# Kernel tuning notes

Hardware: AMD Instinct MI355X
Metric: run time of the kernel (lower is better)

Reference implementation:

```python
import jax, jax.numpy as jnp
import numpy as np

N_NODES = 50000
N_EDGES = 1600000
N_GRAPHS = 512
IN_C, H1, H2, H3, OUT_C = 16, 64, 64, 128, 10


def setup_inputs() -> dict:
    key = jax.random.key(0)
    ks = jax.random.split(key, 12)
    x = jax.random.normal(ks[0], (N_NODES, IN_C), dtype=jnp.float32)
    edge_index = jax.random.randint(ks[1], (2, N_EDGES), 0, N_NODES, dtype=jnp.int64 if jax.config.jax_enable_x64 else jnp.int32)
    batch = jnp.sort(jax.random.randint(ks[2], (N_NODES,), 0, N_GRAPHS))
    s = 0.05
    return {
        "x": x,
        "edge_index": edge_index,
        "batch": batch,
        "W1": jax.random.normal(ks[3], (IN_C, H1), dtype=jnp.float32) * s,
        "b1": jnp.zeros((H1,), jnp.float32),
        "W2": jax.random.normal(ks[4], (H1, H2), dtype=jnp.float32) * s,
        "b2": jnp.zeros((H2,), jnp.float32),
        "Wf1": jax.random.normal(ks[5], (H2, H3), dtype=jnp.float32) * s,
        "bf1": jnp.zeros((H3,), jnp.float32),
        "Wf2": jax.random.normal(ks[6], (H3, OUT_C), dtype=jnp.float32) * s,
        "bf2": jnp.zeros((OUT_C,), jnp.float32),
    }


def reference(x, edge_index, batch, W1, b1, W2, b2, Wf1, bf1, Wf2, bf2):
    N = x.shape[0]
    self_idx = jnp.arange(N, dtype=edge_index.dtype)
    # PyG GCNConv default: add self-loops, symmetric normalization deg^-1/2
    src = jnp.concatenate([edge_index[0], self_idx])
    dst = jnp.concatenate([edge_index[1], self_idx])
    deg = jnp.zeros((N,), x.dtype).at[dst].add(1.0)  # >= 1 due to self-loops
    dinv = jax.lax.rsqrt(deg)
    norm = dinv[src] * dinv[dst]  # [E+N]

    def gcn_conv(h, W, b):
        hw = h @ W                                   # [N, C_out]
        msgs = hw[src] * norm[:, None]               # gather [E+N, C_out]
        return jax.ops.segment_sum(msgs, dst, num_segments=N) + b

    h = jax.nn.relu(gcn_conv(x, W1, b1))
    h = jax.nn.relu(gcn_conv(h, W2, b2))

    # global_mean_pool over graph ids
    counts = jax.ops.segment_sum(jnp.ones((N,), h.dtype), batch, num_segments=N_GRAPHS)
    sums = jax.ops.segment_sum(h, batch, num_segments=N_GRAPHS)
    pooled = sums / jnp.maximum(counts, 1.0)[:, None]  # [G, H2]

    out = pooled @ Wf1 + bf1
    out = out @ Wf2 + bf2
    return out
```

## Files before the change

kernel.cpp:

```cpp
#include <hip/hip_runtime.h>

#define N_NODES   50000
#define N_EDGES   1600000
#define N_GRAPHS  512
#define IN_C      16
#define H1        64
#define H2        64
#define H3        128
#define OUT_C     10

#define NBKT      196
#define CHUNK     4096
#define CAP       12288
#define PLANE_DW  (N_NODES * 16)

typedef unsigned int  uint;
typedef unsigned short ushort;


__global__ void __launch_bounds__(256) k_binB(const int* __restrict__ src,
                                              const int* __restrict__ dst,
                                              int* __restrict__ bkt_fill,
                                              uint* __restrict__ bucket_edges) {
    __shared__ int  lcnt[NBKT];
    __shared__ int  loff[NBKT];
    __shared__ int  gbase[NBKT];
    __shared__ int  tmp[256];
    __shared__ uint stage[CHUNK];
    int tid = threadIdx.x;
    long long e0 = (long long)blockIdx.x * CHUNK;
    int cn = (int)((N_EDGES - e0) < CHUNK ? (N_EDGES - e0) : CHUNK);

    for (int i = tid; i < NBKT; i += 256) lcnt[i] = 0;
    __syncthreads();

    uint pk[16]; int rk[16]; int bkr[16];
#pragma unroll
    for (int k = 0; k < 16; ++k) {
        int i = k * 256 + tid;
        pk[k] = 0; rk[k] = -1; bkr[k] = 0;
        if (i < cn) {
            int e = (int)e0 + i;
            uint d = (uint)dst[e], s = (uint)src[e];
            pk[k] = (d << 16) | s;
            bkr[k] = (int)(d >> 8);
            rk[k] = atomicAdd(&lcnt[bkr[k]], 1);
        }
    }
    __syncthreads();

    int v = (tid < NBKT) ? lcnt[tid] : 0;
    tmp[tid] = v;
    __syncthreads();
    for (int s = 1; s < 256; s <<= 1) {
        int t = (tid >= s) ? tmp[tid - s] : 0;
        __syncthreads();
        tmp[tid] += t;
        __syncthreads();
    }
    if (tid < NBKT) loff[tid] = tmp[tid] - v;
    if (tid < NBKT && v > 0) gbase[tid] = atomicAdd(&bkt_fill[tid], v);
    __syncthreads();

#pragma unroll
    for (int k = 0; k < 16; ++k)
        if (rk[k] >= 0) stage[loff[bkr[k]] + rk[k]] = pk[k];
    __syncthreads();

    for (int i = tid; i < cn; i += 256) {
        uint p = stage[i];
        int b = (int)(p >> 24);
        int pos = gbase[b] + (i - loff[b]);
        if (pos < CAP) bucket_edges[(size_t)b * CAP + pos] = p;
    }
}


__global__ void __launch_bounds__(256) k_bkt_csr(const int* __restrict__ bkt_fill,
                                                 const uint* __restrict__ bucket_edges,
                                                 const float* __restrict__ x,
                                                 int* __restrict__ rowbeg,
                                                 int* __restrict__ rowend,
                                                 float* __restrict__ dinv,
                                                 float* __restrict__ xs,
                                                 ushort* __restrict__ src_sorted,
                                                 float* __restrict__ pool,
                                                 float* __restrict__ gcnt) {
    __shared__ int ncnt[256];
    __shared__ int noff[256];
    __shared__ int tmp[256];
    __shared__ ushort su[CAP];
    int b = blockIdx.x, tid = threadIdx.x;
    int base = b * CAP;
    int cntE = bkt_fill[b];
    if (cntE > CAP) cntE = CAP;

    int gt = b * 256 + tid;
    if (gt < N_GRAPHS * H2) pool[gt] = 0.f;
    if (gt < N_GRAPHS) gcnt[gt] = 0.f;

    ncnt[tid] = 0;
    __syncthreads();
    for (int i = tid; i < cntE; i += 256) {
        uint p = bucket_edges[base + i];
        atomicAdd(&ncnt[(p >> 16) & 255], 1);
    }
    __syncthreads();

    int v = ncnt[tid];
    tmp[tid] = v;
    __syncthreads();
    for (int s = 1; s < 256; s <<= 1) {
        int t = (tid >= s) ? tmp[tid - s] : 0;
        __syncthreads();
        tmp[tid] += t;
        __syncthreads();
    }
    noff[tid] = tmp[tid] - v;

    int n = b * 256 + tid;
    if (n < N_NODES) {
        rowbeg[n] = base + (tmp[tid] - v);
        rowend[n] = base + tmp[tid];
        float dv = rsqrtf((float)(v + 1));
        dinv[n] = dv;
        const float4* xr = (const float4*)(x + (size_t)n * IN_C);
        float4* xo = (float4*)(xs + (size_t)n * IN_C);
#pragma unroll
        for (int j = 0; j < 4; ++j) {
            float4 t = xr[j];
            t.x *= dv; t.y *= dv; t.z *= dv; t.w *= dv;
            xo[j] = t;
        }
    }

    ncnt[tid] = 0;
    __syncthreads();
    for (int i = tid; i < cntE; i += 256) {
        uint p = bucket_edges[base + i];
        int l = (p >> 16) & 255;
        int r = atomicAdd(&ncnt[l], 1);
        int pos = noff[l] + r;
        if (pos < CAP) su[pos] = (ushort)(p & 0xFFFF);
    }
    __syncthreads();
    for (int i = tid; i < cntE; i += 256)
        src_sorted[base + i] = su[i];
}


__device__ __forceinline__ uint f2bf(float f) {
    uint b = __float_as_uint(f);
    return (b + 0x7fffu + ((b >> 16) & 1u)) >> 16;
}

__global__ void __launch_bounds__(256) k_layer1(
    const int* __restrict__ rowbeg, const int* __restrict__ rowend,
    const ushort* __restrict__ src_sorted,
    const float* __restrict__ dinv, const float* __restrict__ xs,
    const float* __restrict__ W1, const float* __restrict__ b1,
    const float* __restrict__ W2, uint* __restrict__ ubf)
{
    __shared__ float W1l[IN_C * 64];
    __shared__ float W2l[H1 * 64];
    __shared__ float axl[32 * 16];
    __shared__ float tl[32 * 64];
    int tid = threadIdx.x;

    ((float4*)W1l)[tid] = ((const float4*)W1)[tid];
#pragma unroll
    for (int i = tid; i < H1 * 16; i += 256)
        ((float4*)W2l)[i] = ((const float4*)W2)[i];

    int ln = tid >> 3;
    int n = blockIdx.x * 32 + ln;
    int sub = tid & 7;
    int slot = sub >> 2;
    int c4 = (sub & 3) << 2;
    bool valid = n < N_NODES;

    int beg = 0, end = 0;
    float di = 0.f;
    if (valid) { beg = rowbeg[n]; end = rowend[n]; di = dinv[n]; }

    float4 acc = {0.f,0.f,0.f,0.f}, acc2 = {0.f,0.f,0.f,0.f};
    if (valid && slot == 0)
        acc = *(const float4*)(xs + (size_t)n * 16 + c4);

    for (int i = beg; i < end; i += 4) {
        int i0 = i + slot, i1 = i0 + 2;
        bool k0 = i0 < end, k1 = i1 < end;
        int s0 = k0 ? (int)src_sorted[i0] : 0;
        int s1 = k1 ? (int)src_sorted[i1] : 0;
        float m0 = k0 ? 1.f : 0.f;
        float m1 = k1 ? 1.f : 0.f;
        float4 h0 = *(const float4*)(xs + (size_t)s0 * 16 + c4);
        float4 h1 = *(const float4*)(xs + (size_t)s1 * 16 + c4);
        acc.x  = fmaf(h0.x, m0, acc.x);   acc.y  = fmaf(h0.y, m0, acc.y);
        acc.z  = fmaf(h0.z, m0, acc.z);   acc.w  = fmaf(h0.w, m0, acc.w);
        acc2.x = fmaf(h1.x, m1, acc2.x);  acc2.y = fmaf(h1.y, m1, acc2.y);
        acc2.z = fmaf(h1.z, m1, acc2.z);  acc2.w = fmaf(h1.w, m1, acc2.w);
    }
    acc.x += acc2.x; acc.y += acc2.y; acc.z += acc2.z; acc.w += acc2.w;
    acc.x += __shfl_xor(acc.x, 4);
    acc.y += __shfl_xor(acc.y, 4);
    acc.z += __shfl_xor(acc.z, 4);
    acc.w += __shfl_xor(acc.w, 4);
    if (slot == 0) {
        acc.x *= di; acc.y *= di; acc.z *= di; acc.w *= di;
        *(float4*)(&axl[ln * 16 + c4]) = acc;
    }
    __syncthreads();

    int c0 = (tid & 7) * 8;
    float a1[8];
#pragma unroll
    for (int j = 0; j < 8; ++j) a1[j] = 0.f;
    const float* an = &axl[ln * 16];
#pragma unroll
    for (int kb = 0; kb < IN_C / 4; ++kb) {
        float4 r = *(const float4*)(an + kb * 4);
        const float* wr = &W1l[(kb * 4) * 64 + c0];
        float rk[4] = {r.x, r.y, r.z, r.w};
#pragma unroll
        for (int k = 0; k < 4; ++k) {
            float4 w0 = *(const float4*)(wr + k * 64);
            float4 w1 = *(const float4*)(wr + k * 64 + 4);
            a1[0] += rk[k] * w0.x;  a1[1] += rk[k] * w0.y;
            a1[2] += rk[k] * w0.z;  a1[3] += rk[k] * w0.w;
            a1[4] += rk[k] * w1.x;  a1[5] += rk[k] * w1.y;
            a1[6] += rk[k] * w1.z;  a1[7] += rk[k] * w1.w;
        }
    }
    float4 bv0 = *(const float4*)(b1 + c0);
    float4 bv1 = *(const float4*)(b1 + c0 + 4);
    float* tr = &tl[ln * 64 + c0];
    tr[0] = fmaxf(a1[0] + bv0.x, 0.f) * di;
    tr[1] = fmaxf(a1[1] + bv0.y, 0.f) * di;
    tr[2] = fmaxf(a1[2] + bv0.z, 0.f) * di;
    tr[3] = fmaxf(a1[3] + bv0.w, 0.f) * di;
    tr[4] = fmaxf(a1[4] + bv1.x, 0.f) * di;
    tr[5] = fmaxf(a1[5] + bv1.y, 0.f) * di;
    tr[6] = fmaxf(a1[6] + bv1.z, 0.f) * di;
    tr[7] = fmaxf(a1[7] + bv1.w, 0.f) * di;
    __syncthreads();

    float u[8];
#pragma unroll
    for (int j = 0; j < 8; ++j) u[j] = 0.f;
    const float* tn = &tl[ln * 64];
#pragma unroll 4
    for (int kb = 0; kb < H1 / 4; ++kb) {
        float4 r = *(const float4*)(tn + kb * 4);
        const float* wr = &W2l[(kb * 4) * 64 + c0];
        float rk[4] = {r.x, r.y, r.z, r.w};
#pragma unroll
        for (int k = 0; k < 4; ++k) {
            float4 w0 = *(const float4*)(wr + k * 64);
            float4 w1 = *(const float4*)(wr + k * 64 + 4);
            u[0] += rk[k] * w0.x;  u[1] += rk[k] * w0.y;
            u[2] += rk[k] * w0.z;  u[3] += rk[k] * w0.w;
            u[4] += rk[k] * w1.x;  u[5] += rk[k] * w1.y;
            u[6] += rk[k] * w1.z;  u[7] += rk[k] * w1.w;
        }
    }
    if (valid) {
        uint4 pk;
        pk.x = f2bf(u[0]) | (f2bf(u[1]) << 16);
        pk.y = f2bf(u[2]) | (f2bf(u[3]) << 16);
        pk.z = f2bf(u[4]) | (f2bf(u[5]) << 16);
        pk.w = f2bf(u[6]) | (f2bf(u[7]) << 16);
        size_t dw = (size_t)(c0 >> 5) * PLANE_DW + (size_t)n * 16 + ((c0 & 31) >> 1);
        *(uint4*)(ubf + dw) = pk;
    }
}


__global__ void __launch_bounds__(256) k_agg32bf(
    const int* __restrict__ rowbeg, const int* __restrict__ rowend,
    const ushort* __restrict__ src_sorted,
    const float* __restrict__ dinv, const uint* __restrict__ ubf,
    const float* __restrict__ b2, float* __restrict__ h2)
{
    int h = (int)(blockIdx.x & 1);
    int nb = (int)(blockIdx.x >> 1);
    int n = nb * 4 + (threadIdx.x >> 6);
    if (n >= N_NODES) return;
    int lane = threadIdx.x & 63;
    int slot = lane >> 2;
    int l4 = lane & 3;
    const uint* up = ubf + (size_t)h * PLANE_DW;
    const uint4* U = (const uint4*)up;

    int beg = rowbeg[n], end = rowend[n];
    float acc[8];
#pragma unroll
    for (int j = 0; j < 8; ++j) acc[j] = 0.f;

    if (slot == 0) {
        uint4 v = U[(size_t)n * 4 + l4];
        uint d[4] = {v.x, v.y, v.z, v.w};
#pragma unroll
        for (int k = 0; k < 4; ++k) {
            acc[2*k]   = __uint_as_float(d[k] << 16);
            acc[2*k+1] = __uint_as_float(d[k] & 0xFFFF0000u);
        }
    }

    for (int i = beg; i < end; i += 32) {
#pragma unroll
        for (int k = 0; k < 2; ++k) {
            int idx = i + slot + 16 * k;
            bool kk = idx < end;
            int s = kk ? (int)src_sorted[idx] : 0;
            float m = kk ? 1.f : 0.f;
            uint4 v = U[(size_t)s * 4 + l4];
            acc[0] = fmaf(__uint_as_float(v.x << 16),         m, acc[0]);
            acc[1] = fmaf(__uint_as_float(v.x & 0xFFFF0000u), m, acc[1]);
            acc[2] = fmaf(__uint_as_float(v.y << 16),         m, acc[2]);
            acc[3] = fmaf(__uint_as_float(v.y & 0xFFFF0000u), m, acc[3]);
            acc[4] = fmaf(__uint_as_float(v.z << 16),         m, acc[4]);
            acc[5] = fmaf(__uint_as_float(v.z & 0xFFFF0000u), m, acc[5]);
            acc[6] = fmaf(__uint_as_float(v.w << 16),         m, acc[6]);
            acc[7] = fmaf(__uint_as_float(v.w & 0xFFFF0000u), m, acc[7]);
        }
    }

#pragma unroll
    for (int off = 4; off <= 32; off <<= 1) {
#pragma unroll
        for (int j = 0; j < 8; ++j)
            acc[j] += __shfl_xor(acc[j], off);
    }

    if (slot == 0) {
        float di = dinv[n];
        int c8 = h * 32 + l4 * 8;
        float4 bv0 = *(const float4*)(b2 + c8);
        float4 bv1 = *(const float4*)(b2 + c8 + 4);
        float4 o0 = {fmaf(acc[0], di, bv0.x), fmaf(acc[1], di, bv0.y),
                     fmaf(acc[2], di, bv0.z), fmaf(acc[3], di, bv0.w)};
        float4 o1 = {fmaf(acc[4], di, bv1.x), fmaf(acc[5], di, bv1.y),
                     fmaf(acc[6], di, bv1.z), fmaf(acc[7], di, bv1.w)};
        *(float4*)(h2 + (size_t)n * 64 + c8)     = o0;
        *(float4*)(h2 + (size_t)n * 64 + c8 + 4) = o1;
    }
}


__global__ void __launch_bounds__(256) k_pool2(const int* __restrict__ batch,
                                               const float* __restrict__ h,
                                               float* __restrict__ pool,
                                               float* __restrict__ gcnt) {
    int wave = (blockIdx.x * blockDim.x + threadIdx.x) >> 6;
    int lane = threadIdx.x & 63;
    int n0 = wave * 64;
    if (n0 >= N_NODES) return;
    int nend = n0 + 64 < N_NODES ? n0 + 64 : N_NODES;
    int g = batch[n0];
    float acc = 0.f, c = 0.f;
    for (int n = n0; n < nend; ++n) {
        int gn = batch[n];
        if (gn != g) {
            atomicAdd(&pool[g * 64 + lane], acc);
            if (lane == 0) atomicAdd(&gcnt[g], c);
            acc = 0.f; c = 0.f; g = gn;
        }
        acc += fmaxf(h[(size_t)n * 64 + lane], 0.f);
        c += 1.f;
    }
    atomicAdd(&pool[g * 64 + lane], acc);
    if (lane == 0) atomicAdd(&gcnt[g], c);
}


__global__ void __launch_bounds__(128)
k_mlp(const float* __restrict__ pool, const float* __restrict__ cnt,
      const float* __restrict__ Wf1, const float* __restrict__ bf1,
      const float* __restrict__ Wf2, const float* __restrict__ bf2,
      float* __restrict__ out) {
    int g = blockIdx.x;
    int tid = threadIdx.x;
    __shared__ float p[H2];
    __shared__ float tbuf[H3];
    float inv = 1.0f / fmaxf(cnt[g], 1.0f);
    if (tid < H2) p[tid] = pool[g * H2 + tid] * inv;
    __syncthreads();
    {
        float acc = bf1[tid];
#pragma unroll
        for (int k = 0; k < H2; ++k) acc += p[k] * Wf1[k * H3 + tid];
        tbuf[tid] = acc;
    }
    __syncthreads();
    if (tid < OUT_C) {
        float acc = bf2[tid];
#pragma unroll
        for (int m = 0; m < H3; ++m) acc += tbuf[m] * Wf2[m * OUT_C + tid];
        out[g * OUT_C + tid] = acc;
    }
}


extern "C" void kernel_launch(void* const* d_in, const int* in_sizes, int n_in,
                              void* d_out, int out_size, void* d_ws, size_t ws_size,
                              hipStream_t stream) {
    const float* x    = (const float*)d_in[0];
    const int*   ei   = (const int*)  d_in[1];
    const int*   batch= (const int*)  d_in[2];
    const float* W1   = (const float*)d_in[3];
    const float* b1   = (const float*)d_in[4];
    const float* W2   = (const float*)d_in[5];
    const float* b2   = (const float*)d_in[6];
    const float* Wf1  = (const float*)d_in[7];
    const float* bf1  = (const float*)d_in[8];
    const float* Wf2  = (const float*)d_in[9];
    const float* bf2  = (const float*)d_in[10];
    float* out = (float*)d_out;

    const int* src = ei;
    const int* dst = ei + N_EDGES;

    char* ws = (char*)d_ws;
    size_t off = 0;
    auto alloc = [&](size_t bytes) {
        char* p = ws + off;
        off += (bytes + 255) & ~size_t(255);
        return p;
    };
    int*    bkt_fill   = (int*)   alloc(NBKT * sizeof(int));
    float*  pool       = (float*) alloc(N_GRAPHS * H2 * sizeof(float));
    float*  gcnt       = (float*) alloc(N_GRAPHS * sizeof(float));
    float*  dinv       = (float*) alloc(N_NODES * sizeof(float));
    int*    rowbeg     = (int*)   alloc(N_NODES * sizeof(int));
    int*    rowend     = (int*)   alloc(N_NODES * sizeof(int));
    ushort* src_sorted = (ushort*)alloc((size_t)NBKT * CAP * sizeof(ushort));
    float*  xs         = (float*) alloc((size_t)N_NODES * IN_C * sizeof(float));
    float*  bufA       = (float*) alloc((size_t)N_NODES * 64 * sizeof(float));
    float*  bufB       = (float*) alloc((size_t)N_NODES * 64 * sizeof(float));
    uint*   bucket_edges = (uint*)bufB;
    uint*   ubf          = (uint*)bufB;
    (void)ws_size;

    const int BLK = 256;
    int gE  = (N_EDGES + CHUNK - 1) / CHUNK;
    int gG  = (N_NODES + 31) / 32;
    int gA  = ((N_NODES + 3) / 4) * 2;
    int gPW = ((N_NODES + 63) / 64 * 64 + BLK - 1) / BLK;

    hipMemsetAsync(bkt_fill, 0, NBKT * sizeof(int), stream);

    k_binB   <<<gE, BLK, 0, stream>>>(src, dst, bkt_fill, bucket_edges);
    k_bkt_csr<<<NBKT, BLK, 0, stream>>>(bkt_fill, bucket_edges, x,
                                        rowbeg, rowend, dinv, xs, src_sorted,
                                        pool, gcnt);

    k_layer1<<<gG, BLK, 0, stream>>>(rowbeg, rowend, src_sorted, dinv, xs,
                                     W1, b1, W2, ubf);

    k_agg32bf<<<gA, BLK, 0, stream>>>(rowbeg, rowend, src_sorted, dinv, ubf, b2, bufA);

    k_pool2<<<gPW, BLK, 0, stream>>>(batch, bufA, pool, gcnt);
    k_mlp  <<<N_GRAPHS, 128, 0, stream>>>(pool, gcnt, Wf1, bf1, Wf2, bf2, out);
}
```

Measured before the change: 155.9 us.

## Fuse layer-2 aggregation with mean pooling and use a single bf16 plane layout

Merges the second aggregation kernel with global mean pooling: each node's ReLU output is atomically added straight into the per-graph pool, so the fp32 h2 buffer and the separate pool kernel go away. The bf16 hidden features are stored as one 64-wide row per node instead of two 32-column planes, so a single wave gathers all columns. Pool and count zeroing moves into one memset, and graph counts are accumulated with atomics during CSR building. In exchange, pooling now issues many more contended float atomics per node, and atomic ordering makes the summation order nondeterministic.

Result: slower. 270.7 us (+73.6%).

```diff
diff --git a/kernel.cpp b/kernel.cpp
--- a/kernel.cpp
+++ b/kernel.cpp
@@ -79,12 +79,12 @@
 __global__ void __launch_bounds__(256) k_bkt_csr(const int* __restrict__ bkt_fill,
                                                  const uint* __restrict__ bucket_edges,
                                                  const float* __restrict__ x,
+                                                 const int* __restrict__ batch,
                                                  int* __restrict__ rowbeg,
                                                  int* __restrict__ rowend,
                                                  float* __restrict__ dinv,
                                                  float* __restrict__ xs,
                                                  ushort* __restrict__ src_sorted,
-                                                 float* __restrict__ pool,
                                                  float* __restrict__ gcnt) {
     __shared__ int ncnt[256];
     __shared__ int noff[256];
@@ -95,10 +95,6 @@
     int cntE = bkt_fill[b];
     if (cntE > CAP) cntE = CAP;
 
-    int gt = b * 256 + tid;
-    if (gt < N_GRAPHS * H2) pool[gt] = 0.f;
-    if (gt < N_GRAPHS) gcnt[gt] = 0.f;
-
     ncnt[tid] = 0;
     __syncthreads();
     for (int i = tid; i < cntE; i += 256) {
@@ -124,6 +120,7 @@
         rowend[n] = base + tmp[tid];
         float dv = rsqrtf((float)(v + 1));
         dinv[n] = dv;
+        atomicAdd(&gcnt[batch[n]], 1.0f);
         const float4* xr = (const float4*)(x + (size_t)n * IN_C);
         float4* xo = (float4*)(xs + (size_t)n * IN_C);
 #pragma unroll
@@ -270,27 +267,24 @@
         pk.y = f2bf(u[2]) | (f2bf(u[3]) << 16);
         pk.z = f2bf(u[4]) | (f2bf(u[5]) << 16);
         pk.w = f2bf(u[6]) | (f2bf(u[7]) << 16);
-        size_t dw = (size_t)(c0 >> 5) * PLANE_DW + (size_t)n * 16 + ((c0 & 31) >> 1);
-        *(uint4*)(ubf + dw) = pk;
-    }
-}
-
-
-__global__ void __launch_bounds__(256) k_agg32bf(
+        ((uint4*)ubf)[(size_t)n * 8 + (tid & 7)] = pk;
+    }
+}
+
+
+__global__ void __launch_bounds__(256) k_aggpool(
     const int* __restrict__ rowbeg, const int* __restrict__ rowend,
     const ushort* __restrict__ src_sorted,
     const float* __restrict__ dinv, const uint* __restrict__ ubf,
-    const float* __restrict__ b2, float* __restrict__ h2)
+    const float* __restrict__ b2, const int* __restrict__ batch,
+    float* __restrict__ pool)
 {
-    int h = (int)(blockIdx.x & 1);
-    int nb = (int)(blockIdx.x >> 1);
-    int n = nb * 4 + (threadIdx.x >> 6);
+    int n = (int)(blockIdx.x * 4 + (threadIdx.x >> 6));
     if (n >= N_NODES) return;
     int lane = threadIdx.x & 63;
-    int slot = lane >> 2;
-    int l4 = lane & 3;
-    const uint* up = ubf + (size_t)h * PLANE_DW;
-    const uint4* U = (const uint4*)up;
+    int slot = lane >> 3;
+    int l8 = lane & 7;
+    const uint4* U = (const uint4*)ubf;
 
     int beg = rowbeg[n], end = rowend[n];
     float acc[8];
@@ -298,7 +292,7 @@
     for (int j = 0; j < 8; ++j) acc[j] = 0.f;
 
     if (slot == 0) {
-        uint4 v = U[(size_t)n * 4 + l4];
+        uint4 v = U[(size_t)n * 8 + l8];
         uint d[4] = {v.x, v.y, v.z, v.w};
 #pragma unroll
         for (int k = 0; k < 4; ++k) {
@@ -309,12 +303,12 @@
 
     for (int i = beg; i < end; i += 32) {
 #pragma unroll
-        for (int k = 0; k < 2; ++k) {
-            int idx = i + slot + 16 * k;
+        for (int k = 0; k < 4; ++k) {
+            int idx = i + slot + 8 * k;
             bool kk = idx < end;
             int s = kk ? (int)src_sorted[idx] : 0;
             float m = kk ? 1.f : 0.f;
-            uint4 v = U[(size_t)s * 4 + l4];
+            uint4 v = U[(size_t)s * 8 + l8];
             acc[0] = fmaf(__uint_as_float(v.x << 16),         m, acc[0]);
             acc[1] = fmaf(__uint_as_float(v.x & 0xFFFF0000u), m, acc[1]);
             acc[2] = fmaf(__uint_as_float(v.y << 16),         m, acc[2]);
@@ -327,7 +321,7 @@
     }
 
 #pragma unroll
-    for (int off = 4; off <= 32; off <<= 1) {
+    for (int off = 8; off <= 32; off <<= 1) {
 #pragma unroll
         for (int j = 0; j < 8; ++j)
             acc[j] += __shfl_xor(acc[j], off);
@@ -335,42 +329,20 @@
 
     if (slot == 0) {
         float di = dinv[n];
-        int c8 = h * 32 + l4 * 8;
+        int g = batch[n];
+        int c8 = l8 * 8;
         float4 bv0 = *(const float4*)(b2 + c8);
         float4 bv1 = *(const float4*)(b2 + c8 + 4);
-        float4 o0 = {fmaf(acc[0], di, bv0.x), fmaf(acc[1], di, bv0.y),
-                     fmaf(acc[2], di, bv0.z), fmaf(acc[3], di, bv0.w)};
-        float4 o1 = {fmaf(acc[4], di, bv1.x), fmaf(acc[5], di, bv1.y),
-                     fmaf(acc[6], di, bv1.z), fmaf(acc[7], di, bv1.w)};
-        *(float4*)(h2 + (size_t)n * 64 + c8)     = o0;
-        *(float4*)(h2 + (size_t)n * 64 + c8 + 4) = o1;
-    }
-}
-
-
-__global__ void __launch_bounds__(256) k_pool2(const int* __restrict__ batch,
-                                               const float* __restrict__ h,
-                                               float* __restrict__ pool,
-                                               float* __restrict__ gcnt) {
-    int wave = (blockIdx.x * blockDim.x + threadIdx.x) >> 6;
-    int lane = threadIdx.x & 63;
-    int n0 = wave * 64;
-    if (n0 >= N_NODES) return;
-    int nend = n0 + 64 < N_NODES ? n0 + 64 : N_NODES;
-    int g = batch[n0];
-    float acc = 0.f, c = 0.f;
-    for (int n = n0; n < nend; ++n) {
-        int gn = batch[n];
-        if (gn != g) {
-            atomicAdd(&pool[g * 64 + lane], acc);
-            if (lane == 0) atomicAdd(&gcnt[g], c);
-            acc = 0.f; c = 0.f; g = gn;
-        }
-        acc += fmaxf(h[(size_t)n * 64 + lane], 0.f);
-        c += 1.f;
-    }
-    atomicAdd(&pool[g * 64 + lane], acc);
-    if (lane == 0) atomicAdd(&gcnt[g], c);
+        float* pr = pool + (size_t)g * 64 + c8;
+        atomicAdd(pr + 0, fmaxf(fmaf(acc[0], di, bv0.x), 0.f));
+        atomicAdd(pr + 1, fmaxf(fmaf(acc[1], di, bv0.y), 0.f));
+        atomicAdd(pr + 2, fmaxf(fmaf(acc[2], di, bv0.z), 0.f));
+        atomicAdd(pr + 3, fmaxf(fmaf(acc[3], di, bv0.w), 0.f));
+        atomicAdd(pr + 4, fmaxf(fmaf(acc[4], di, bv1.x), 0.f));
+        atomicAdd(pr + 5, fmaxf(fmaf(acc[5], di, bv1.y), 0.f));
+        atomicAdd(pr + 6, fmaxf(fmaf(acc[6], di, bv1.z), 0.f));
+        atomicAdd(pr + 7, fmaxf(fmaf(acc[7], di, bv1.w), 0.f));
+    }
 }
 
 
@@ -431,35 +403,33 @@
     int*    bkt_fill   = (int*)   alloc(NBKT * sizeof(int));
     float*  pool       = (float*) alloc(N_GRAPHS * H2 * sizeof(float));
     float*  gcnt       = (float*) alloc(N_GRAPHS * sizeof(float));
+    size_t  zero_bytes = off;
     float*  dinv       = (float*) alloc(N_NODES * sizeof(float));
     int*    rowbeg     = (int*)   alloc(N_NODES * sizeof(int));
     int*    rowend     = (int*)   alloc(N_NODES * sizeof(int));
     ushort* src_sorted = (ushort*)alloc((size_t)NBKT * CAP * sizeof(ushort));
     float*  xs         = (float*) alloc((size_t)N_NODES * IN_C * sizeof(float));
-    float*  bufA       = (float*) alloc((size_t)N_NODES * 64 * sizeof(float));
     float*  bufB       = (float*) alloc((size_t)N_NODES * 64 * sizeof(float));
     uint*   bucket_edges = (uint*)bufB;
     uint*   ubf          = (uint*)bufB;
     (void)ws_size;
 
     const int BLK = 256;
-    int gE  = (N_EDGES + CHUNK - 1) / CHUNK;
-    int gG  = (N_NODES + 31) / 32;
-    int gA  = ((N_NODES + 3) / 4) * 2;
-    int gPW = ((N_NODES + 63) / 64 * 64 + BLK - 1) / BLK;
-
-    hipMemsetAsync(bkt_fill, 0, NBKT * sizeof(int), stream);
+    int gE = (N_EDGES + CHUNK - 1) / CHUNK;
+    int gG = (N_NODES + 31) / 32;
+    int gA = (N_NODES + 3) / 4;
+
+    hipMemsetAsync(bkt_fill, 0, zero_bytes, stream);
 
     k_binB   <<<gE, BLK, 0, stream>>>(src, dst, bkt_fill, bucket_edges);
-    k_bkt_csr<<<NBKT, BLK, 0, stream>>>(bkt_fill, bucket_edges, x,
-                                        rowbeg, rowend, dinv, xs, src_sorted,
-                                        pool, gcnt);
+    k_bkt_csr<<<NBKT, BLK, 0, stream>>>(bkt_fill, bucket_edges, x, batch,
+                                        rowbeg, rowend, dinv, xs, src_sorted, gcnt);
 
     k_layer1<<<gG, BLK, 0, stream>>>(rowbeg, rowend, src_sorted, dinv, xs,
                                      W1, b1, W2, ubf);
 
-    k_agg32bf<<<gA, BLK, 0, stream>>>(rowbeg, rowend, src_sorted, dinv, ubf, b2, bufA);
-
-    k_pool2<<<gPW, BLK, 0, stream>>>(batch, bufA, pool, gcnt);
-    k_mlp  <<<N_GRAPHS, 128, 0, stream>>>(pool, gcnt, Wf1, bf1, Wf2, bf2, out);
-}
+    k_aggpool<<<gA, BLK, 0, stream>>>(rowbeg, rowend, src_sorted, dinv, ubf,
+                                      b2, batch, pool);
+
+    k_mlp<<<N_GRAPHS, 128, 0, stream>>>(pool, gcnt, Wf1, bf1, Wf2, bf2, out);
+}
```

## Use interleaved 64-channel bf16 layout and single-pass aggregation; stage bucket edges in LDS

Applied to the files above, without the earlier changes.

Changes the bf16 intermediate from two 32-channel planes to one interleaved 128-byte row per node. The aggregation kernel now covers all 64 channels with one wave per node, 8 lanes per row and 8 edge slots, which halves the gather launches and the index and rowbeg reads. The CSR builder keeps bucket edges in LDS instead of reading them twice from global memory, and scatters src_sorted directly to global rather than through an LDS copy. Pool and count zeroing moves into the existing memset. Each wave now handles fewer concurrent edges per node, which may reduce memory-level parallelism, and the direct scatter drops the CAP bounds check.

Result: faster. 139.9 us (median of 2 runs) (-10.3%).

```diff
diff --git a/kernel.cpp b/kernel.cpp
--- a/kernel.cpp
+++ b/kernel.cpp
@@ -12,7 +12,6 @@
 #define NBKT      196
 #define CHUNK     4096
 #define CAP       12288
-#define PLANE_DW  (N_NODES * 16)
 
 typedef unsigned int  uint;
 typedef unsigned short ushort;
@@ -83,26 +82,21 @@
                                                  int* __restrict__ rowend,
                                                  float* __restrict__ dinv,
                                                  float* __restrict__ xs,
-                                                 ushort* __restrict__ src_sorted,
-                                                 float* __restrict__ pool,
-                                                 float* __restrict__ gcnt) {
+                                                 ushort* __restrict__ src_sorted) {
+    __shared__ uint stageE[CAP];
     __shared__ int ncnt[256];
     __shared__ int noff[256];
     __shared__ int tmp[256];
-    __shared__ ushort su[CAP];
     int b = blockIdx.x, tid = threadIdx.x;
     int base = b * CAP;
     int cntE = bkt_fill[b];
     if (cntE > CAP) cntE = CAP;
 
-    int gt = b * 256 + tid;
-    if (gt < N_GRAPHS * H2) pool[gt] = 0.f;
-    if (gt < N_GRAPHS) gcnt[gt] = 0.f;
-
     ncnt[tid] = 0;
     __syncthreads();
     for (int i = tid; i < cntE; i += 256) {
         uint p = bucket_edges[base + i];
+        stageE[i] = p;
         atomicAdd(&ncnt[(p >> 16) & 255], 1);
     }
     __syncthreads();
@@ -137,15 +131,11 @@
     ncnt[tid] = 0;
     __syncthreads();
     for (int i = tid; i < cntE; i += 256) {
-        uint p = bucket_edges[base + i];
+        uint p = stageE[i];
         int l = (p >> 16) & 255;
         int r = atomicAdd(&ncnt[l], 1);
-        int pos = noff[l] + r;
-        if (pos < CAP) su[pos] = (ushort)(p & 0xFFFF);
-    }
-    __syncthreads();
-    for (int i = tid; i < cntE; i += 256)
-        src_sorted[base + i] = su[i];
+        src_sorted[base + noff[l] + r] = (ushort)(p & 0xFFFF);
+    }
 }
 
 
@@ -270,27 +260,23 @@
         pk.y = f2bf(u[2]) | (f2bf(u[3]) << 16);
         pk.z = f2bf(u[4]) | (f2bf(u[5]) << 16);
         pk.w = f2bf(u[6]) | (f2bf(u[7]) << 16);
-        size_t dw = (size_t)(c0 >> 5) * PLANE_DW + (size_t)n * 16 + ((c0 & 31) >> 1);
-        *(uint4*)(ubf + dw) = pk;
-    }
-}
-
-
-__global__ void __launch_bounds__(256) k_agg32bf(
+        ((uint4*)ubf)[(size_t)n * 8 + (tid & 7)] = pk;
+    }
+}
+
+
+__global__ void __launch_bounds__(256) k_agg64bf(
     const int* __restrict__ rowbeg, const int* __restrict__ rowend,
     const ushort* __restrict__ src_sorted,
     const float* __restrict__ dinv, const uint* __restrict__ ubf,
     const float* __restrict__ b2, float* __restrict__ h2)
 {
-    int h = (int)(blockIdx.x & 1);
-    int nb = (int)(blockIdx.x >> 1);
-    int n = nb * 4 + (threadIdx.x >> 6);
+    int n = (int)(blockIdx.x * 4 + (threadIdx.x >> 6));
     if (n >= N_NODES) return;
     int lane = threadIdx.x & 63;
-    int slot = lane >> 2;
-    int l4 = lane & 3;
-    const uint* up = ubf + (size_t)h * PLANE_DW;
-    const uint4* U = (const uint4*)up;
+    int slot = lane >> 3;
+    int l8 = lane & 7;
+    const uint4* U = (const uint4*)ubf;
 
     int beg = rowbeg[n], end = rowend[n];
     float acc[8];
@@ -298,7 +284,7 @@
     for (int j = 0; j < 8; ++j) acc[j] = 0.f;
 
     if (slot == 0) {
-        uint4 v = U[(size_t)n * 4 + l4];
+        uint4 v = U[(size_t)n * 8 + l8];
         uint d[4] = {v.x, v.y, v.z, v.w};
 #pragma unroll
         for (int k = 0; k < 4; ++k) {
@@ -309,12 +295,12 @@
 
     for (int i = beg; i < end; i += 32) {
 #pragma unroll
-        for (int k = 0; k < 2; ++k) {
-            int idx = i + slot + 16 * k;
+        for (int k = 0; k < 4; ++k) {
+            int idx = i + slot + 8 * k;
             bool kk = idx < end;
             int s = kk ? (int)src_sorted[idx] : 0;
             float m = kk ? 1.f : 0.f;
-            uint4 v = U[(size_t)s * 4 + l4];
+            uint4 v = U[(size_t)s * 8 + l8];
             acc[0] = fmaf(__uint_as_float(v.x << 16),         m, acc[0]);
             acc[1] = fmaf(__uint_as_float(v.x & 0xFFFF0000u), m, acc[1]);
             acc[2] = fmaf(__uint_as_float(v.y << 16),         m, acc[2]);
@@ -327,7 +313,7 @@
     }
 
 #pragma unroll
-    for (int off = 4; off <= 32; off <<= 1) {
+    for (int off = 8; off <= 32; off <<= 1) {
 #pragma unroll
         for (int j = 0; j < 8; ++j)
             acc[j] += __shfl_xor(acc[j], off);
@@ -335,7 +321,7 @@
 
     if (slot == 0) {
         float di = dinv[n];
-        int c8 = h * 32 + l4 * 8;
+        int c8 = l8 * 8;
         float4 bv0 = *(const float4*)(b2 + c8);
         float4 bv1 = *(const float4*)(b2 + c8 + 4);
         float4 o0 = {fmaf(acc[0], di, bv0.x), fmaf(acc[1], di, bv0.y),
@@ -431,6 +417,7 @@
     int*    bkt_fill   = (int*)   alloc(NBKT * sizeof(int));
     float*  pool       = (float*) alloc(N_GRAPHS * H2 * sizeof(float));
     float*  gcnt       = (float*) alloc(N_GRAPHS * sizeof(float));
+    size_t  zero_bytes = off;
     float*  dinv       = (float*) alloc(N_NODES * sizeof(float));
     int*    rowbeg     = (int*)   alloc(N_NODES * sizeof(int));
     int*    rowend     = (int*)   alloc(N_NODES * sizeof(int));
@@ -445,20 +432,19 @@
     const int BLK = 256;
     int gE  = (N_EDGES + CHUNK - 1) / CHUNK;
     int gG  = (N_NODES + 31) / 32;
-    int gA  = ((N_NODES + 3) / 4) * 2;
+    int gA  = (N_NODES + 3) / 4;
     int gPW = ((N_NODES + 63) / 64 * 64 + BLK - 1) / BLK;
 
-    hipMemsetAsync(bkt_fill, 0, NBKT * sizeof(int), stream);
+    hipMemsetAsync(bkt_fill, 0, zero_bytes, stream);
 
     k_binB   <<<gE, BLK, 0, stream>>>(src, dst, bkt_fill, bucket_edges);
     k_bkt_csr<<<NBKT, BLK, 0, stream>>>(bkt_fill, bucket_edges, x,
-                                        rowbeg, rowend, dinv, xs, src_sorted,
-                                        pool, gcnt);
+                                        rowbeg, rowend, dinv, xs, src_sorted);
 
     k_layer1<<<gG, BLK, 0, stream>>>(rowbeg, rowend, src_sorted, dinv, xs,
                                      W1, b1, W2, ubf);
 
-    k_agg32bf<<<gA, BLK, 0, stream>>>(rowbeg, rowend, src_sorted, dinv, ubf, b2, bufA);
+    k_agg64bf<<<gA, BLK, 0, stream>>>(rowbeg, rowend, src_sorted, dinv, ubf, b2, bufA);
 
     k_pool2<<<gPW, BLK, 0, stream>>>(batch, bufA, pool, gcnt);
     k_mlp  <<<N_GRAPHS, 128, 0, stream>>>(pool, gcnt, Wf1, bf1, Wf2, bf2, out);
```
